# Kernel tuning notes

Hardware: AMD Instinct MI355X
Metric: run time of the kernel (lower is better)

## Reference

```python
import jax, jax.numpy as jnp
import numpy as np

HEAD_NUM = 16

def setup_inputs() -> dict:
    key = jax.random.key(0)
    k1, k2 = jax.random.split(key)
    bs, seq, d = 2, 2048, 1024
    embeddings = jax.random.normal(k1, (bs, seq, d), dtype=jnp.float32)
    W = jax.random.normal(k2, (d, 3 * d), dtype=jnp.float32) * (1.0 / np.sqrt(d))
    b = jnp.zeros((3 * d,), dtype=jnp.float32)
    return {"embeddings": embeddings, "W": W, "b": b}

def reference(embeddings, W, b):
    bs, seq, d = embeddings.shape
    h = HEAD_NUM
    qkv = embeddings @ W + b                      # [b, s, 3d]
    q, k, v = jnp.split(qkv, 3, axis=-1)          # each [b, s, d]
    hd = d // h
    # Faithful to source: reshape to (bs, seq, head_dim, heads) then permute
    def split_heads(x, head_dim):
        return x.reshape(bs, seq, head_dim, h).transpose(0, 3, 1, 2)  # [b, h, s, hd]
    mq = split_heads(q, hd)
    mk = split_heads(k, hd)
    mv = split_heads(v, hd)
    scale = jnp.sqrt(jnp.asarray(hd, dtype=mq.dtype))
    scores = jnp.einsum('bhqd,bhkd->bhqk', mq, mk) / scale  # [b, h, s, s]
    attn = jax.nn.softmax(scores, axis=-1)
    out = jnp.einsum('bhqk,bhkv->bhqv', attn, mv)            # [b, h, s, hd]
    return out.transpose(0, 2, 1, 3).reshape(bs, seq, -1)    # [b, s, d]
```

## Files before the change

kernel.cpp:

```cpp
#include <hip/hip_runtime.h>
#include <stdint.h>

typedef unsigned short u16;
typedef unsigned int u32;
typedef float f32x4 __attribute__((ext_vector_type(4)));
typedef __bf16 bf16x8 __attribute__((ext_vector_type(8)));

#define BS 2
#define SEQ 2048
#define DIM 1024
#define NW3 3072
#define NH 16
#define HD 64

#define MFMA_BF16(a, b, c) __builtin_amdgcn_mfma_f32_16x16x32_bf16((a), (b), (c), 0, 0, 0)

#define GLL16(g, l)                                                                \
  __builtin_amdgcn_global_load_lds(                                                \
      (__attribute__((address_space(1))) void*)(void*)(uintptr_t)(g),              \
      (__attribute__((address_space(3))) void*)(l), 16, 0, 0)

__device__ __forceinline__ float fexp2(float x) {
#if defined(__has_builtin)
#if __has_builtin(__builtin_amdgcn_exp2f)
  return __builtin_amdgcn_exp2f(x);
#else
  return exp2f(x);
#endif
#else
  return exp2f(x);
#endif
}

__device__ __forceinline__ u16 f2bf(float x) {
  __bf16 h = (__bf16)x;
  return __builtin_bit_cast(u16, h);
}

#define CSC 0.18033688011112042f

__global__ __launch_bounds__(256) void conv_kernel(const float* __restrict__ A,
                                                   u16* __restrict__ O,
                                                   const float* __restrict__ W,
                                                   u16* __restrict__ Wt) {
  if (blockIdx.x < 4096) {
    int i = (blockIdx.x * 256 + threadIdx.x) * 4;
    float4 v = *(const float4*)(A + i);
    union { u16 u[4]; ushort4 v4; } p;
    p.u[0] = f2bf(v.x); p.u[1] = f2bf(v.y); p.u[2] = f2bf(v.z); p.u[3] = f2bf(v.w);
    *(ushort4*)(O + i) = p.v4;
  } else {
    int id = (blockIdx.x - 4096) * 256 + threadIdx.x;
    int kc = id / NW3;
    int n = id - kc * NW3;
    union { u16 u[8]; uint4 v; } p;
#pragma unroll
    for (int i = 0; i < 8; ++i) p.u[i] = f2bf(W[(kc * 8 + i) * NW3 + n]);
    int h = n & 15, hd = (n & 1023) >> 4;
    int np = (n & ~1023) + h * 64 + hd;
    *(uint4*)(Wt + np * DIM + kc * 8) = p.v;
  }
}

#define GSTAGE(ADST, BDST, KT)                                                 \
  {                                                                            \
    const int koff = (KT) * 64;                                \
    _Pragma("unroll") for (int r = 0; r < 2; ++r) {                            \
      int l = r * 256 + t;                            \
      int row = l >> 2, pos = l & 3;                                           \
      int kc = pos ^ (row & 3);                                                \
      GLL16(Abase + row * 2048 + koff + kc * 16, (char*)(ADST) + l * 16);      \
      GLL16(Bbase + row * 2048 + koff + kc * 16, (char*)(BDST) + l * 16);      \
    }                                                                          \
  }

#define GCOMPUTE(AT, BT)                                                       \
  {                                                                            \
    bf16x8 af[4], bfr[4];                                                      \
    _Pragma("unroll") for (int mt = 0; mt < 4; ++mt) {                         \
      int row = wm + mt * 16 + c;                                              \
      int kc = quad ^ (row & 3);                                               \
      af[mt] = *(const bf16x8*)((const char*)(AT) + row * 64 + kc * 16);       \
    }                                                                          \
    _Pragma("unroll") for (int nt = 0; nt < 4; ++nt) {                         \
      int row = wn + nt * 16 + c;                                              \
      int kc = quad ^ (row & 3);                                               \
      bfr[nt] = *(const bf16x8*)((const char*)(BT) + row * 64 + kc * 16);      \
    }                                                                          \
    _Pragma("unroll") for (int mt = 0; mt < 4; ++mt)                           \
      _Pragma("unroll") for (int nt = 0; nt < 4; ++nt)                         \
        acc[mt][nt] = MFMA_BF16(af[mt], bfr[nt], acc[mt][nt]);                 \
  }

__global__ __launch_bounds__(256) void gemm_qkv_kernel(
    const u16* __restrict__ Ab, const u16* __restrict__ Bt, const float* __restrict__ bias,
    u16* __restrict__ Q, u16* __restrict__ K, u16* __restrict__ Vt) {
  __shared__ __align__(16) u16 Aa[128 * 32];
  __shared__ __align__(16) u16 Ab2[128 * 32];
  __shared__ __align__(16) u16 Ba[128 * 32];
  __shared__ __align__(16) u16 Bb2[128 * 32];
  const int t = threadIdx.x;
  const int lane = t & 63, wave = t >> 6;
  const int c = lane & 15, quad = lane >> 4;
  const int tm = blockIdx.x / 24, tn = blockIdx.x - tm * 24;
  const int wm = (wave >> 1) * 64, wn = (wave & 1) * 64;

  const char* Abase = (const char*)(Ab + (size_t)tm * 128 * DIM);
  const char* Bbase = (const char*)(Bt + (size_t)tn * 128 * DIM);

  f32x4 z = {0.f, 0.f, 0.f, 0.f};
  f32x4 acc[4][4];
#pragma unroll
  for (int i = 0; i < 4; ++i)
#pragma unroll
    for (int j = 0; j < 4; ++j) acc[i][j] = z;

  GSTAGE(Aa, Ba, 0);
  __syncthreads();
  for (int kt = 0; kt < 32; kt += 2) {
    GSTAGE(Ab2, Bb2, kt + 1);
    GCOMPUTE(Aa, Ba);
    __syncthreads();
    if (kt + 2 < 32) GSTAGE(Aa, Ba, kt + 2);
    GCOMPUTE(Ab2, Bb2);
    __syncthreads();
  }

#pragma unroll
  for (int nt = 0; nt < 4; ++nt) {
    int np = tn * 128 + wn + nt * 16 + c;
    int which = np >> 10;
    int rem = np & 1023;
    int h = rem >> 6, hd = rem & 63;
    float bv = bias[(np & ~1023) + hd * 16 + h];
    float sc = (which == 0) ? CSC : 1.0f;
    float bvs = bv * sc;
#pragma unroll
    for (int mt = 0; mt < 4; ++mt) {
      int mbase = tm * 128 + wm + mt * 16 + quad * 4;
      int bI = mbase >> 11;
      int s0 = mbase & 2047;
      if (which == 2) {
        union { u16 u[4]; uint2 v; } p;
#pragma unroll
        for (int r = 0; r < 4; ++r) p.u[r] = f2bf(acc[mt][nt][r] + bv);
        *(uint2*)(Vt + ((size_t)(bI * NH + h) * HD + hd) * SEQ + s0) = p.v;
      } else {
        u16* dst = (which == 0) ? Q : K;
#pragma unroll
        for (int r = 0; r < 4; ++r)
          dst[((size_t)(bI * NH + h) * SEQ + (s0 + r)) * HD + hd] =
              f2bf(acc[mt][nt][r] * sc + bvs);
      }
    }
  }
}

#define STAGE_KV(KDST, VDST, KTILE)                                            \
  {                                                                            \
    const char* Ktb = Kb + (size_t)(KTILE) * 8192;        \
    const char* Vtb = Vb + (size_t)(KTILE) * 128;         \
    _Pragma("unroll") for (int r = 0; r < 2; ++r) {                            \
      int l = r * 256 + t;                                                     \
      int row = l >> 3, pos = l & 7;                                           \
      int kc = pos ^ (row & 7);                                                \
      GLL16(Ktb + row * 128 + kc * 16, (char*)(KDST) + l * 16);                \
      GLL16(Vtb + row * 4096 + kc * 16, (char*)(VDST) + l * 16);               \
    }                                                                          \
  }

#define COMPUTE_TILE(KT, VT)                                                   \
  {                                                                            \
    f32x4 sT[4];                                                               \
    _Pragma("unroll") for (int mt = 0; mt < 4; ++mt) {                         \
      sT[mt] = z;                                                              \
      _Pragma("unroll") for (int ks = 0; ks < 2; ++ks) {                       \
        int row = mt * 16 + c;                                                 \
        int kc = (ks * 4 + quad) ^ (row & 7);                                  \
        bf16x8 kf = *(const bf16x8*)((const char*)(KT) + row * 128 + kc * 16); \
        sT[mt] = MFMA_BF16(kf, qf[ks], sT[mt]);                                \
      }                                                                        \
    }                                                                          \
    u32 pk[4][2];                                                              \
    _Pragma("unroll") for (int mt = 0; mt < 4; ++mt) {                         \
      float p0 = fexp2(sT[mt][0]);                                             \
      float p1 = fexp2(sT[mt][1]);                                             \
      float p2 = fexp2(sT[mt][2]);                                             \
      float p3 = fexp2(sT[mt][3]);                                             \
      sm0 += p0; sm1 += p1; sm2 += p2; sm3 += p3;                              \
      pk[mt][0] = (u32)f2bf(p0) | ((u32)f2bf(p1) << 16);                       \
      pk[mt][1] = (u32)f2bf(p2) | ((u32)f2bf(p3) << 16);                       \
    }                                                                          \
    _Pragma("unroll") for (int ks = 0; ks < 2; ++ks) {                         \
      u32 a0 = __shfl(pk[2 * ks][0], sl0), a1 = __shfl(pk[2 * ks][1], sl0);    \
      u32 a2 = __shfl(pk[2 * ks][0], sl1), a3 = __shfl(pk[2 * ks][1], sl1);    \
      u32 b0 = __shfl(pk[2 * ks + 1][0], sl0);                                 \
      u32 b1 = __shfl(pk[2 * ks + 1][1], sl0);                                 \
      u32 b2 = __shfl(pk[2 * ks + 1][0], sl1);                                 \
      u32 b3 = __shfl(pk[2 * ks + 1][1], sl1);                                 \
      uint4 wv;                                                                \
      wv.x = hi ? b0 : a0; wv.y = hi ? b1 : a1;                                \
      wv.z = hi ? b2 : a2; wv.w = hi ? b3 : a3;                                \
      bf16x8 pf = __builtin_bit_cast(bf16x8, wv);                              \
      _Pragma("unroll") for (int mt = 0; mt < 4; ++mt) {                       \
        int row = mt * 16 + c;                                                 \
        int kc = (ks * 4 + quad) ^ (row & 7);                                  \
        bf16x8 vf = *(const bf16x8*)((const char*)(VT) + row * 128 + kc * 16); \
        accO[mt] = MFMA_BF16(vf, pf, accO[mt]);                                \
      }                                                                        \
    }                                                                          \
  }

__global__ __launch_bounds__(256, 4) void attn_kernel(
    const u16* __restrict__ Q, const u16* __restrict__ K,
    const u16* __restrict__ Vt, float* __restrict__ Out) {
  __shared__ __align__(16) u16 Ka[64 * 64];
  __shared__ __align__(16) u16 Kb2[64 * 64];
  __shared__ __align__(16) u16 Va[64 * 64];
  __shared__ __align__(16) u16 Vb2[64 * 64];
  const int t = threadIdx.x;
  const int lane = t & 63, wave = t >> 6;
  const int c = lane & 15, quad = lane >> 4;
  const int qt = blockIdx.x & 31, bh = blockIdx.x >> 5;
  const int h = bh & 15, b = bh >> 4;

  const u16* Qb = Q + ((size_t)bh * SEQ + qt * 64) * HD;
  const char* Kb = (const char*)(K + (size_t)bh * SEQ * HD);
  const char* Vb = (const char*)(Vt + (size_t)bh * HD * SEQ);

#pragma unroll
  for (int r = 0; r < 2; ++r) {
    int l = r * 256 + t;
    int row = l >> 3, pos = l & 7;
    int kc = pos ^ (row & 7);
    GLL16((const char*)Qb + row * 128 + kc * 16, (char*)Ka + l * 16);
  }
  __syncthreads();
  bf16x8 qf[2];
#pragma unroll
  for (int ks = 0; ks < 2; ++ks) {
    int row = wave * 16 + c;
    int kc = (ks * 4 + quad) ^ (row & 7);
    qf[ks] = *(const bf16x8*)((const char*)Ka + row * 128 + kc * 16);
  }
  __syncthreads();

  float sm0 = 0.f, sm1 = 0.f, sm2 = 0.f, sm3 = 0.f;
  f32x4 z = {0.f, 0.f, 0.f, 0.f};
  f32x4 accO[4];
#pragma unroll
  for (int i = 0; i < 4; ++i) accO[i] = z;

  const int sl0 = c + 16 * ((quad & 1) * 2);
  const int sl1 = sl0 + 16;
  const bool hi = quad >= 2;

  STAGE_KV(Ka, Va, 0);
  __syncthreads();

  for (int kt = 0; kt < 32; kt += 2) {
    STAGE_KV(Kb2, Vb2, kt + 1);
    COMPUTE_TILE(Ka, Va);
    __syncthreads();
    if (kt + 2 < 32) STAGE_KV(Ka, Va, kt + 2);
    COMPUTE_TILE(Kb2, Vb2);
    __syncthreads();
  }

  float l = (sm0 + sm1) + (sm2 + sm3);
  l += __shfl_xor(l, 16);
  l += __shfl_xor(l, 32);
  float inv = 1.f / l;
  int s = qt * 64 + wave * 16 + c;
#pragma unroll
  for (int mt = 0; mt < 4; ++mt) {
    float4 o;
    o.x = accO[mt][0] * inv;
    o.y = accO[mt][1] * inv;
    o.z = accO[mt][2] * inv;
    o.w = accO[mt][3] * inv;
    size_t off = ((size_t)(b * SEQ + s)) * DIM + h * HD + mt * 16 + quad * 4;
    *(float4*)(Out + off) = o;
  }
}

extern "C" void kernel_launch(void* const* d_in, const int* in_sizes, int n_in,
                              void* d_out, int out_size, void* d_ws, size_t ws_size,
                              hipStream_t stream) {
  (void)in_sizes; (void)n_in; (void)out_size; (void)ws_size;
  const float* emb = (const float*)d_in[0];
  const float* W = (const float*)d_in[1];
  const float* bias = (const float*)d_in[2];
  float* out = (float*)d_out;
  char* ws = (char*)d_ws;
  u16* Ab = (u16*)ws;
  u16* Wt = (u16*)(ws + 8388608);
  u16* Qd = (u16*)(ws + 14680064);
  u16* Kd = (u16*)(ws + 23068672);
  u16* Vd = (u16*)(ws + 31457280);

  conv_kernel<<<5632, 256, 0, stream>>>(emb, Ab, W, Wt);
  gemm_qkv_kernel<<<768, 256, 0, stream>>>(Ab, Wt, bias, Qd, Kd, Vd);
  attn_kernel<<<1024, 256, 0, stream>>>(Qd, Kd, Vd, out);
}
```

Before: 179.1 us.

## Split attention waves across query pairs and key halves with LDS reduction

The 4 waves are reorganized as 2 query groups × 2 key-halves. Each wave computes 32 queries against 32 of the 64 keys per tile, so every K and V fragment read from LDS feeds two MFMAs instead of one. The partial O accumulators and row sums from the two key-half waves are combined through shared memory at the end. This cuts LDS read traffic and shuffles per MFMA, at the cost of more accumulator registers and an extra reduction and sync in the epilogue.

```diff
diff --git a/kernel.cpp b/kernel.cpp
--- a/kernel.cpp
+++ b/kernel.cpp
@@ -171,43 +171,44 @@
 
 #define COMPUTE_TILE(KT, VT)                                                   \
   {                                                                            \
-    f32x4 sT[4];                                                               \
-    _Pragma("unroll") for (int mt = 0; mt < 4; ++mt) {                         \
-      sT[mt] = z;                                                              \
+    f32x4 sT[2][2]; \
+    sT[0][0] = z; sT[0][1] = z; sT[1][0] = z; sT[1][1] = z;                    \
+    _Pragma("unroll") for (int mt2 = 0; mt2 < 2; ++mt2) {                      \
       _Pragma("unroll") for (int ks = 0; ks < 2; ++ks) {                       \
-        int row = mt * 16 + c;                                                 \
+        int row = ws * 32 + mt2 * 16 + c;                                      \
         int kc = (ks * 4 + quad) ^ (row & 7);                                  \
         bf16x8 kf = *(const bf16x8*)((const char*)(KT) + row * 128 + kc * 16); \
-        sT[mt] = MFMA_BF16(kf, qf[ks], sT[mt]);                                \
+        sT[mt2][0] = MFMA_BF16(kf, qf[0][ks], sT[mt2][0]);                     \
+        sT[mt2][1] = MFMA_BF16(kf, qf[1][ks], sT[mt2][1]);                     \
       }                                                                        \
     }                                                                          \
-    u32 pk[4][2];                                                              \
-    _Pragma("unroll") for (int mt = 0; mt < 4; ++mt) {                         \
-      float p0 = fexp2(sT[mt][0]);                                             \
-      float p1 = fexp2(sT[mt][1]);                                             \
-      float p2 = fexp2(sT[mt][2]);                                             \
-      float p3 = fexp2(sT[mt][3]);                                             \
-      sm0 += p0; sm1 += p1; sm2 += p2; sm3 += p3;                              \
-      pk[mt][0] = (u32)f2bf(p0) | ((u32)f2bf(p1) << 16);                       \
-      pk[mt][1] = (u32)f2bf(p2) | ((u32)f2bf(p3) << 16);                       \
-    }                                                                          \
-    _Pragma("unroll") for (int ks = 0; ks < 2; ++ks) {                         \
-      u32 a0 = __shfl(pk[2 * ks][0], sl0), a1 = __shfl(pk[2 * ks][1], sl0);    \
-      u32 a2 = __shfl(pk[2 * ks][0], sl1), a3 = __shfl(pk[2 * ks][1], sl1);    \
-      u32 b0 = __shfl(pk[2 * ks + 1][0], sl0);                                 \
-      u32 b1 = __shfl(pk[2 * ks + 1][1], sl0);                                 \
-      u32 b2 = __shfl(pk[2 * ks + 1][0], sl1);                                 \
-      u32 b3 = __shfl(pk[2 * ks + 1][1], sl1);                                 \
+    bf16x8 pf[2];                                                              \
+    _Pragma("unroll") for (int nt = 0; nt < 2; ++nt) {                         \
+      u32 pk[2][2];                                                            \
+      _Pragma("unroll") for (int mt2 = 0; mt2 < 2; ++mt2) {                    \
+        float p0 = fexp2(sT[mt2][nt][0]);                                      \
+        float p1 = fexp2(sT[mt2][nt][1]);                                      \
+        float p2 = fexp2(sT[mt2][nt][2]);                                      \
+        float p3 = fexp2(sT[mt2][nt][3]);                                      \
+        smA[nt] += p0 + p1; smB[nt] += p2 + p3;                                \
+        pk[mt2][0] = (u32)f2bf(p0) | ((u32)f2bf(p1) << 16);                    \
+        pk[mt2][1] = (u32)f2bf(p2) | ((u32)f2bf(p3) << 16);                    \
+      }                                                                        \
+      u32 a0 = __shfl(pk[0][0], sl0), a1 = __shfl(pk[0][1], sl0);              \
+      u32 a2 = __shfl(pk[0][0], sl1), a3 = __shfl(pk[0][1], sl1);              \
+      u32 b0 = __shfl(pk[1][0], sl0), b1 = __shfl(pk[1][1], sl0);              \
+      u32 b2 = __shfl(pk[1][0], sl1), b3 = __shfl(pk[1][1], sl1);              \
       uint4 wv;                                                                \
       wv.x = hi ? b0 : a0; wv.y = hi ? b1 : a1;                                \
       wv.z = hi ? b2 : a2; wv.w = hi ? b3 : a3;                                \
-      bf16x8 pf = __builtin_bit_cast(bf16x8, wv);                              \
-      _Pragma("unroll") for (int mt = 0; mt < 4; ++mt) {                       \
-        int row = mt * 16 + c;                                                 \
-        int kc = (ks * 4 + quad) ^ (row & 7);                                  \
-        bf16x8 vf = *(const bf16x8*)((const char*)(VT) + row * 128 + kc * 16); \
-        accO[mt] = MFMA_BF16(vf, pf, accO[mt]);                                \
-      }                                                                        \
+      pf[nt] = __builtin_bit_cast(bf16x8, wv);                                 \
+    }                                                                          \
+    _Pragma("unroll") for (int mt = 0; mt < 4; ++mt) {                         \
+      int row = mt * 16 + c;                                                   \
+      int kc = vq ^ (row & 7);                                                 \
+      bf16x8 vf = *(const bf16x8*)((const char*)(VT) + row * 128 + kc * 16);   \
+      accO[mt][0] = MFMA_BF16(vf, pf[0], accO[mt][0]);                         \
+      accO[mt][1] = MFMA_BF16(vf, pf[1], accO[mt][1]);                         \
     }                                                                          \
   }
 
@@ -221,6 +222,7 @@
   const int t = threadIdx.x;
   const int lane = t & 63, wave = t >> 6;
   const int c = lane & 15, quad = lane >> 4;
+  const int wq = wave & 1, ws = wave >> 1;
   const int qt = blockIdx.x & 31, bh = blockIdx.x >> 5;
   const int h = bh & 15, b = bh >> 4;
 
@@ -236,24 +238,27 @@
     GLL16((const char*)Qb + row * 128 + kc * 16, (char*)Ka + l * 16);
   }
   __syncthreads();
-  bf16x8 qf[2];
-#pragma unroll
-  for (int ks = 0; ks < 2; ++ks) {
-    int row = wave * 16 + c;
-    int kc = (ks * 4 + quad) ^ (row & 7);
-    qf[ks] = *(const bf16x8*)((const char*)Ka + row * 128 + kc * 16);
-  }
-  __syncthreads();
-
-  float sm0 = 0.f, sm1 = 0.f, sm2 = 0.f, sm3 = 0.f;
+  bf16x8 qf[2][2];
+#pragma unroll
+  for (int nt = 0; nt < 2; ++nt)
+#pragma unroll
+    for (int ks = 0; ks < 2; ++ks) {
+      int row = wq * 32 + nt * 16 + c;
+      int kc = (ks * 4 + quad) ^ (row & 7);
+      qf[nt][ks] = *(const bf16x8*)((const char*)Ka + row * 128 + kc * 16);
+    }
+  __syncthreads();
+
+  float smA[2] = {0.f, 0.f}, smB[2] = {0.f, 0.f};
   f32x4 z = {0.f, 0.f, 0.f, 0.f};
-  f32x4 accO[4];
-#pragma unroll
-  for (int i = 0; i < 4; ++i) accO[i] = z;
+  f32x4 accO[4][2];
+#pragma unroll
+  for (int i = 0; i < 4; ++i) { accO[i][0] = z; accO[i][1] = z; }
 
   const int sl0 = c + 16 * ((quad & 1) * 2);
   const int sl1 = sl0 + 16;
   const bool hi = quad >= 2;
+  const int vq = ws * 4 + quad;
 
   STAGE_KV(Ka, Va, 0);
   __syncthreads();
@@ -267,20 +272,51 @@
     __syncthreads();
   }
 
-  float l = (sm0 + sm1) + (sm2 + sm3);
-  l += __shfl_xor(l, 16);
-  l += __shfl_xor(l, 32);
-  float inv = 1.f / l;
-  int s = qt * 64 + wave * 16 + c;
-#pragma unroll
-  for (int mt = 0; mt < 4; ++mt) {
-    float4 o;
-    o.x = accO[mt][0] * inv;
-    o.y = accO[mt][1] * inv;
-    o.z = accO[mt][2] * inv;
-    o.w = accO[mt][3] * inv;
-    size_t off = ((size_t)(b * SEQ + s)) * DIM + h * HD + mt * 16 + quad * 4;
-    *(float4*)(Out + off) = o;
+  float sm[2];
+#pragma unroll
+  for (int nt = 0; nt < 2; ++nt) {
+    float s = smA[nt] + smB[nt];
+    s += __shfl_xor(s, 16);
+    s += __shfl_xor(s, 32);
+    sm[nt] = s;
+  }
+  if (ws == 1) {
+    float* fb = (float*)(wq ? (void*)Kb2 : (void*)Ka);
+#pragma unroll
+    for (int mt = 0; mt < 4; ++mt)
+#pragma unroll
+      for (int nt = 0; nt < 2; ++nt)
+        *(f32x4*)(fb + (mt * 2 + nt) * 256 + lane * 4) = accO[mt][nt];
+    float* lb = (float*)Va + wq * 128;
+    lb[lane * 2] = sm[0];
+    lb[lane * 2 + 1] = sm[1];
+  }
+  __syncthreads();
+  if (ws == 0) {
+    const float* fb = (const float*)(wq ? (void*)Kb2 : (void*)Ka);
+#pragma unroll
+    for (int mt = 0; mt < 4; ++mt)
+#pragma unroll
+      for (int nt = 0; nt < 2; ++nt)
+        accO[mt][nt] += *(const f32x4*)(fb + (mt * 2 + nt) * 256 + lane * 4);
+    const float* lb = (const float*)Va + wq * 128;
+    float inv0 = 1.f / (sm[0] + lb[lane * 2]);
+    float inv1 = 1.f / (sm[1] + lb[lane * 2 + 1]);
+    int s0 = qt * 64 + wq * 32 + c;
+#pragma unroll
+    for (int mt = 0; mt < 4; ++mt) {
+#pragma unroll
+      for (int nt = 0; nt < 2; ++nt) {
+        float inv = nt ? inv1 : inv0;
+        float4 o;
+        o.x = accO[mt][nt][0] * inv;
+        o.y = accO[mt][nt][1] * inv;
+        o.z = accO[mt][nt][2] * inv;
+        o.w = accO[mt][nt][3] * inv;
+        size_t off = ((size_t)(b * SEQ + s0 + nt * 16)) * DIM + h * HD + mt * 16 + quad * 4;
+        *(float4*)(Out + off) = o;
+      }
+    }
   }
 }
 
```

Result: faster. 174.6 us (-2.5%).
